# Performance work log

Measured on AMD Instinct MI355X. Metric: run time of the kernel, lower is better.

Reference implementation:

```python
import jax, jax.numpy as jnp
import numpy as np

E = 8        # num_experts
H = 2048     # hidden_size
I = 1408     # expert_intermediate_size
SI = 2816    # shared intermediate = I * num_shared_experts
K = 2        # top_k


def swiglu(x):
    a, b = jnp.split(x, 2, axis=-1)
    return jax.nn.silu(a) * b


def setup_inputs() -> dict:
    key = jax.random.key(0)
    ks = jax.random.split(key, 8)
    hidden_states = jax.random.normal(ks[0], (2, 2048, H), dtype=jnp.float32)
    topk_weight = jax.random.uniform(ks[1], (2, 2048, K), dtype=jnp.float32)
    topk_idx = jax.random.randint(ks[2], (2, 2048, K), 0, E)
    s = 0.02
    W1 = jax.random.normal(ks[3], (E, H, 2 * I), dtype=jnp.float32) * s   # per-expert h->2i (swiglu)
    W2 = jax.random.normal(ks[4], (E, I, H), dtype=jnp.float32) * s      # per-expert i->h
    Ws1 = jax.random.normal(ks[5], (H, 2 * SI), dtype=jnp.float32) * s   # shared h->2*si
    Ws2 = jax.random.normal(ks[6], (SI, H), dtype=jnp.float32) * s       # shared si->h
    return {"hidden_states": hidden_states, "topk_weight": topk_weight,
            "W1": W1, "W2": W2, "Ws1": Ws1, "Ws2": Ws2, "topk_idx": topk_idx}


def reference(hidden_states, topk_weight, W1, W2, Ws1, Ws2, topk_idx):
    orig_shape = hidden_states.shape
    x = hidden_states.reshape(-1, H)                       # [T, h]
    T = x.shape[0]
    # run every expert on every token (dense, faithful to masked-loop math)
    h1 = jnp.einsum('th,ehf->tef', x, W1)                  # [T, E, 2i]
    act = swiglu(h1)                                       # [T, E, i]
    expert_out = jnp.einsum('tei,eih->teh', act, W2)       # [T, E, h]
    # combine weights: comb[t,e] = sum_j topk_weight[t,j] * 1[topk_idx[t,j]==e]
    onehot = jax.nn.one_hot(topk_idx.reshape(T, K), E, dtype=x.dtype)  # [T, K, E]
    comb = jnp.einsum('tk,tke->te', topk_weight.reshape(T, K), onehot)
    y = jnp.einsum('te,teh->th', comb, expert_out)         # [T, h]
    # shared experts MLP on identity
    y = y + swiglu(x @ Ws1) @ Ws2
    return y.reshape(orig_shape)
```

## Files before the change

kernel.cpp:

```cpp
#include <hip/hip_runtime.h>
#include <cmath>

#define E_    8
#define H_    2048
#define IH    1408
#define I2    2816
#define SIH   2816
#define SI2   5632
#define KTOP  2
#define T_    4096
#define NA    (T_*KTOP)
#define MAXR  (NA + E_*256)

typedef __attribute__((ext_vector_type(4)))  short  short4v;
typedef __attribute__((ext_vector_type(8)))  __bf16 bf16x8;
typedef __attribute__((ext_vector_type(4)))  float  f32x4;
typedef unsigned short bf16r;

__device__ __forceinline__ bf16r f2b(float f) {
    unsigned int u = __float_as_uint(f);
    return (bf16r)((u + 0x7FFFu + ((u >> 16) & 1u)) >> 16);
}
__device__ __forceinline__ float b2f(bf16r s) {
    return __uint_as_float(((unsigned int)s) << 16);
}

__device__ __forceinline__ void gld16(const bf16r* g, void* l) {
    __builtin_amdgcn_global_load_lds((const __attribute__((address_space(1))) void*)g,
                                     (__attribute__((address_space(3))) void*)l, 16, 0, 0);
}
__device__ __forceinline__ void barrier_raw() { asm volatile("s_barrier" ::: "memory"); }
template<int N> __device__ __forceinline__ void vmwait() {
    asm volatile("s_waitcnt vmcnt(%0)" :: "i"(N) : "memory");
}

__global__ void route_k(const int* __restrict__ idx, const float* __restrict__ tw,
                        int* __restrict__ route) {
    __shared__ int cnt[E_], cur[E_], offs[E_ + 1];
    int t = threadIdx.x;
    if (t < E_) { cnt[t] = 0; cur[t] = 0; }
    float* wrow = (float*)(route + 64 + MAXR);
    int* pos = route + 64 + 2 * MAXR;
    for (int i = t; i < MAXR; i += 256) { route[64 + i] = -1; wrow[i] = 0.f; }
    __syncthreads();
    for (int a = t; a < NA; a += 256) atomicAdd(&cnt[idx[a]], 1);
    __syncthreads();
    if (t == 0) {
        int run = 0;
        for (int e = 0; e < E_; e++) { offs[e] = run; run += ((cnt[e] + 255) >> 8) << 8; }
        offs[E_] = run;
    }
    __syncthreads();
    for (int a = t; a < NA; a += 256) {
        int e = idx[a];
        int p = atomicAdd(&cur[e], 1);
        int r = offs[e] + p;
        route[64 + r] = a / KTOP;
        wrow[r] = tw[a];
        pos[a] = r;
    }
    if (t <= E_) route[32 + t] = offs[t];
}

__global__ void cvt_k(const float* __restrict__ in, bf16r* __restrict__ out, int n4) {
    int i = blockIdx.x * 256 + threadIdx.x;
    if (i < n4) {
        float4 v = ((const float4*)in)[i];
        short4v o;
        o[0] = (short)f2b(v.x); o[1] = (short)f2b(v.y);
        o[2] = (short)f2b(v.z); o[3] = (short)f2b(v.w);
        ((short4v*)out)[i] = o;
    }
}

__global__ void tconv_k(const float* __restrict__ in, bf16r* __restrict__ out,
                        int R, int C, long ims, long oms) {
    __shared__ bf16r tile[64][65];
    const float* inp = in + blockIdx.z * ims;
    bf16r* outp = out + blockIdx.z * oms;
    int c0 = blockIdx.x * 64, r0 = blockIdx.y * 64;
    int tx = threadIdx.x, ty = threadIdx.y;
    #pragma unroll
    for (int j = 0; j < 16; j++) {
        int r = ty * 16 + j;
        tile[r][tx] = f2b(inp[(long)(r0 + r) * C + c0 + tx]);
    }
    __syncthreads();
    #pragma unroll
    for (int j = 0; j < 16; j++) {
        int c = ty * 16 + j;
        outp[(long)(c0 + c) * R + r0 + tx] = tile[tx][c];
    }
}

__global__ void comb_k(float* __restrict__ out, const bf16r* __restrict__ outR,
                       const int* __restrict__ pos) {
    int i = blockIdx.x * 256 + threadIdx.x;
    int t  = i >> 9;
    int c4 = i & 511;
    int p0 = pos[2 * t], p1 = pos[2 * t + 1];
    float4 o = ((float4*)out)[i];
    short4v r0 = ((const short4v*)(outR + (long)p0 * H_))[c4];
    short4v r1 = ((const short4v*)(outR + (long)p1 * H_))[c4];
    o.x += b2f((bf16r)r0[0]) + b2f((bf16r)r1[0]);
    o.y += b2f((bf16r)r0[1]) + b2f((bf16r)r1[1]);
    o.z += b2f((bf16r)r0[2]) + b2f((bf16r)r1[2]);
    o.w += b2f((bf16r)r0[3]) + b2f((bf16r)r1[3]);
    ((float4*)out)[i] = o;
}


#define PH_READ_A(MH) { _Pragma("unroll") for (int i4 = 0; i4 < 4; i4++) \
                        _Pragma("unroll") for (int kk = 0; kk < 2; kk++) \
                            af[(MH)][i4][kk] = rdA(cur, (MH), i4, kk); }
#define PH_READ_B(NH) { _Pragma("unroll") for (int j2 = 0; j2 < NJ2; j2++) \
                        _Pragma("unroll") for (int kk = 0; kk < 2; kk++) \
                            bfr[(NH)][j2][kk] = rdB(cur, (NH), j2, kk); }
#define PH_MMA(MH, NH) { __builtin_amdgcn_s_setprio(1); \
    _Pragma("unroll") for (int i4 = 0; i4 < 4; i4++) \
    _Pragma("unroll") for (int j2 = 0; j2 < NJ2; j2++) \
    _Pragma("unroll") for (int kk = 0; kk < 2; kk++) \
        acc[(MH)][(NH)][i4][j2] = __builtin_amdgcn_mfma_f32_16x16x32_bf16( \
            af[(MH)][i4][kk], bfr[(NH)][j2][kk], acc[(MH)][(NH)][i4][j2], 0, 0, 0); \
    __builtin_amdgcn_s_setprio(0); }

template<int BNv, int KD, bool GATHER, bool ROUTED, bool PAIRED, int EPI>
__global__ __launch_bounds__(512, 2)
void g8_k(const bf16r* __restrict__ A,
          const bf16r* __restrict__ Bt, long bstride, int F,
          void* __restrict__ Cv, int ldc,
          const int* __restrict__ off, const int* __restrict__ perm,
          const float* __restrict__ wrow, int gM)
{
    constexpr int NJ2 = BNv / 128;
    constexpr int LB  = NJ2;
    constexpr int BHE = BNv * 32;
    constexpr int NT  = KD / 64;
    constexpr int VW  = 4 + 2 * LB;
    static_assert(!PAIRED || NJ2 == 2, "paired swiglu needs BN=256");
    static_assert(NT >= 4 && (NT & 1) == 0, "even K-tile count >= 4");

    extern __shared__ __align__(16) char smem[];
    bf16r* lA = (bf16r*)smem;
    bf16r* lB = (bf16r*)(smem + 65536);

    int nwg = gridDim.x, orig = blockIdx.x;
    int q8 = nwg >> 3, r8 = nwg & 7, xc = orig & 7, o8 = orig >> 3;
    int wgid = (xc < r8 ? xc * (q8 + 1) : r8 * (q8 + 1) + (xc - r8) * q8) + o8;
    int mt = wgid % gM, nt = wgid / gM;
    const int r0 = mt * 256;
    int e = 0;
    if (ROUTED) {
        if (r0 >= off[E_]) return;
        while (e + 1 < E_ && off[e + 1] <= r0) e++;
    }
    const bf16r* Bte = ROUTED ? Bt + (long)e * bstride : Bt;

    const int tid  = threadIdx.x;
    const int lane = tid & 63;
    const int wave = tid >> 6;
    const int wm = wave >> 2, wn = wave & 3;
    const int ml = lane & 15, kg = lane >> 4;
    const int srw  = lane >> 3;
    const int ksrc = ((lane & 7) ^ srw) * 8;

    const bf16r* pA[2][2];
    #pragma unroll
    for (int h = 0; h < 2; h++)
        #pragma unroll
        for (int l = 0; l < 2; l++) {
            int gr = r0 + h * 128 + (wave + 8 * l) * 8 + srw;
            long rw = gr;
            if (GATHER) { int tk = perm[gr]; rw = (tk < 0) ? 0 : tk; }
            pA[h][l] = A + rw * (long)KD + ksrc;
        }
    const bf16r* pB[2][LB];
    #pragma unroll
    for (int nh = 0; nh < 2; nh++)
        #pragma unroll
        for (int l = 0; l < LB; l++) {
            int lr = (wave + 8 * l) * 8 + srw;
            long gr;
            if (PAIRED) {
                int wn_ = lr >> 5, j2_ = (lr >> 4) & 1, ml_ = lr & 15;
                gr = (long)(nt * 128 + nh * 64 + wn_ * 16 + ml_) + (j2_ ? (long)F : 0L);
            } else if (NJ2 == 2) gr = (long)(nt * 256 + nh * 128 + lr);
            else                 gr = (long)(nt * 128 + nh * 64  + lr);
            pB[nh][l] = Bte + gr * (long)KD + ksrc;
        }

    auto stgA = [&](int b, int h, int kp) {
        char* d = smem + ((b * 2 + h) << 14) + (wave << 10);
        gld16(pA[h][0] + kp, d);
        gld16(pA[h][1] + kp, d + 8192);
    };
    auto stgB = [&](int b, int nh, int kp) {
        char* d = smem + 65536 + (b * 2 + nh) * (BHE * 2) + (wave << 10);
        gld16(pB[nh][0] + kp, d);
        if constexpr (LB == 2) gld16(pB[nh][1] + kp, d + 8192);
    };
    auto rdA = [&](int b, int mh, int i4, int kk) -> bf16x8 {
        int row = wm * 64 + i4 * 16 + ml;
        int u = kk * 4 + kg;
        int ee = ((b * 2 + mh) << 13) + row * 64 + ((u ^ (row & 7)) << 3);
        return *(const bf16x8*)&lA[ee];
    };
    auto rdB = [&](int b, int nh, int j2, int kk) -> bf16x8 {
        int rb = (NJ2 == 2) ? (wn * 32 + j2 * 16 + ml) : (wn * 16 + ml);
        int u = kk * 4 + kg;
        int ee = (b * 2 + nh) * BHE + rb * 64 + ((u ^ (rb & 7)) << 3);
        return *(const bf16x8*)&lB[ee];
    };

    f32x4 acc[2][2][4][NJ2];
    #pragma unroll
    for (int a0 = 0; a0 < 2; a0++)
        #pragma unroll
        for (int b0 = 0; b0 < 2; b0++)
            #pragma unroll
            for (int i = 0; i < 4; i++)
                #pragma unroll
                for (int j = 0; j < NJ2; j++)
                    acc[a0][b0][i][j] = f32x4{0.f, 0.f, 0.f, 0.f};

    bf16x8 af[2][4][2], bfr[2][NJ2][2];

    vmwait<0>();
    stgA(0, 0, 0); stgB(0, 0, 0); stgB(0, 1, 0); stgA(0, 1, 0);
    stgA(1, 0, 64); stgB(1, 0, 64);
    vmwait<LB + 2>(); barrier_raw();

    #pragma unroll 2
    for (int t = 0; t < NT; t++) {
        const int cur = t & 1, nxt = cur ^ 1;
        const int k1 = ((t + 1 < NT) ? (t + 1) : (NT - 1)) * 64;
        const int k2 = ((t + 2 < NT) ? (t + 2) : (NT - 1)) * 64;
        PH_READ_A(0); PH_READ_B(0);
        stgB(nxt, 1, k1);
        vmwait<VW>();
        barrier_raw();
        PH_MMA(0, 0);
        barrier_raw();
        PH_READ_B(1);
        stgA(nxt, 1, k1);
        vmwait<VW>();
        barrier_raw();
        PH_MMA(0, 1);
        barrier_raw();
        PH_READ_A(1);
        stgA(cur, 0, k2);
        barrier_raw();
        PH_MMA(1, 0);
        barrier_raw();
        stgB(cur, 0, k2);
        vmwait<VW>();
        barrier_raw();
        PH_MMA(1, 1);
        barrier_raw();
    }
    vmwait<0>();

    const long colbase = (long)nt * (PAIRED ? 128 : BNv);
    #pragma unroll
    for (int mh = 0; mh < 2; mh++)
        #pragma unroll
        for (int i4 = 0; i4 < 4; i4++)
            #pragma unroll
            for (int rr = 0; rr < 4; rr++) {
                long row = (long)r0 + mh * 128 + wm * 64 + i4 * 16 + kg * 4 + rr;
                if constexpr (PAIRED) {
                    bf16r* ap = (bf16r*)Cv + row * (long)ldc + colbase;
                    #pragma unroll
                    for (int nh = 0; nh < 2; nh++) {
                        float g = acc[mh][nh][i4][0][rr];
                        float u = acc[mh][nh][i4][1][rr];
                        float s = g / (1.0f + __expf(-g));
                        ap[nh * 64 + wn * 16 + ml] = f2b(s * u);
                    }
                } else if constexpr (EPI == 1) {
                    float* cp = (float*)Cv + row * (long)ldc + colbase;
                    #pragma unroll
                    for (int nh = 0; nh < 2; nh++)
                        #pragma unroll
                        for (int j2 = 0; j2 < NJ2; j2++)
                            cp[nh * (BNv / 2) + wn * (BNv / 8) + j2 * 16 + ml] =
                                acc[mh][nh][i4][j2][rr];
                } else {
                    int tok = perm[row];
                    if (tok >= 0) {
                        float w = wrow[row];
                        bf16r* cp = (bf16r*)Cv + row * (long)ldc + colbase;
                        #pragma unroll
                        for (int nh = 0; nh < 2; nh++)
                            #pragma unroll
                            for (int j2 = 0; j2 < NJ2; j2++)
                                cp[nh * (BNv / 2) + wn * (BNv / 8) + j2 * 16 + ml] =
                                    f2b(w * acc[mh][nh][i4][j2][rr]);
                    }
                }
            }
}

#undef PH_READ_A
#undef PH_READ_B
#undef PH_MMA

extern "C" void kernel_launch(void* const* d_in, const int* in_sizes, int n_in,
                              void* d_out, int out_size, void* d_ws, size_t ws_size,
                              hipStream_t stream)
{
    const float* x   = (const float*)d_in[0];
    const float* tw  = (const float*)d_in[1];
    const float* W1  = (const float*)d_in[2];
    const float* W2  = (const float*)d_in[3];
    const float* Ws1 = (const float*)d_in[4];
    const float* Ws2 = (const float*)d_in[5];
    const int*   tix = (const int*)d_in[6];
    float* out = (float*)d_out;

    char* ws    = (char*)d_ws;
    int*  route = (int*)ws;
    const int*   off  = route + 32;
    const int*   perm = route + 64;
    const float* wrow = (const float*)(route + 64 + MAXR);
    const int*   pos  = route + 64 + 2 * MAXR;

    bf16r* xb   = (bf16r*)(ws + (1u << 20));
    bf16r* W1t  = xb   + (size_t)T_ * H_;
    bf16r* W2t  = W1t  + (size_t)E_ * I2 * H_;
    bf16r* Ws1t = W2t  + (size_t)E_ * H_ * IH;
    bf16r* Ws2t = Ws1t + (size_t)SI2 * H_;
    bf16r* actS = Ws2t + (size_t)H_ * SIH;
    bf16r* actR = actS + (size_t)T_ * SIH;
    bf16r* outR = W1t;

    static bool attr_done = false;
    if (!attr_done) {
        hipFuncSetAttribute(reinterpret_cast<const void*>(&g8_k<256,2048,false,false,true,0>),
                            hipFuncAttributeMaxDynamicSharedMemorySize, 131072);
        hipFuncSetAttribute(reinterpret_cast<const void*>(&g8_k<256,2048,true,true,true,0>),
                            hipFuncAttributeMaxDynamicSharedMemorySize, 131072);
        hipFuncSetAttribute(reinterpret_cast<const void*>(&g8_k<128,2816,false,false,false,1>),
                            hipFuncAttributeMaxDynamicSharedMemorySize, 98304);
        hipFuncSetAttribute(reinterpret_cast<const void*>(&g8_k<256,1408,false,true,false,2>),
                            hipFuncAttributeMaxDynamicSharedMemorySize, 131072);
        attr_done = true;
    }

    route_k<<<1, 256, 0, stream>>>(tix, tw, route);

    cvt_k<<<(T_ * H_ / 4 + 255) / 256, 256, 0, stream>>>(x, xb, T_ * H_ / 4);
    tconv_k<<<dim3(SI2 / 64, H_ / 64, 1), dim3(64, 4), 0, stream>>>(Ws1, Ws1t, H_, SI2, 0, 0);
    tconv_k<<<dim3(H_ / 64, SIH / 64, 1), dim3(64, 4), 0, stream>>>(Ws2, Ws2t, SIH, H_, 0, 0);
    tconv_k<<<dim3(I2 / 64, H_ / 64, E_), dim3(64, 4), 0, stream>>>(W1, W1t, H_, I2,
                                                                    (long)H_ * I2, (long)I2 * H_);
    tconv_k<<<dim3(H_ / 64, IH / 64, E_), dim3(64, 4), 0, stream>>>(W2, W2t, IH, H_,
                                                                    (long)IH * H_, (long)H_ * IH);

    g8_k<256,2048,false,false,true,0><<<dim3((SIH/128)*(T_/256)), dim3(512), 131072, stream>>>(
        xb, Ws1t, 0, SIH, actS, SIH, nullptr, nullptr, nullptr, T_/256);
    g8_k<128,2816,false,false,false,1><<<dim3((H_/128)*(T_/256)), dim3(512), 98304, stream>>>(
        actS, Ws2t, 0, 0, out, H_, nullptr, nullptr, nullptr, T_/256);
    g8_k<256,2048,true,true,true,0><<<dim3((IH/128)*(MAXR/256)), dim3(512), 131072, stream>>>(
        xb, W1t, (long)I2 * H_, IH, actR, IH, off, perm, nullptr, MAXR/256);
    g8_k<256,1408,false,true,false,2><<<dim3((H_/256)*(MAXR/256)), dim3(512), 131072, stream>>>(
        actR, W2t, (long)H_ * IH, 0, outR, H_, off, perm, wrow, MAXR/256);
    comb_k<<<T_ * H_ / 4 / 256, 256, 0, stream>>>(out, outR, pos);
}
```

Baseline: 816.7 us.

## Merge shared and routed GEMMs into combined launches; vectorize weight transpose

Fuses the shared-expert and routed-expert GEMMs of each stage into a single grid launch that branches on block index, so the two independent problems fill the GPU together and launch gaps disappear. The weight transpose-convert kernel is rewritten to use float4 loads and 16-byte bf16 stores with a padded tile. Routing and gather flags become runtime values, and the block-swizzle formula drops its remainder handling, which assumes each grid count is a multiple of 8. The shared second GEMM now requests the larger 128KB LDS budget, which may limit occupancy.

```diff
diff --git a/kernel.cpp b/kernel.cpp
--- a/kernel.cpp
+++ b/kernel.cpp
@@ -11,6 +11,11 @@
 #define T_    4096
 #define NA    (T_*KTOP)
 #define MAXR  (NA + E_*256)
+
+#define NS1   ((SIH/128)*(T_/256))
+#define NR1   ((IH/128)*(MAXR/256))
+#define NS2   ((H_/128)*(T_/256))
+#define NR2   ((H_/256)*(MAXR/256))
 
 typedef __attribute__((ext_vector_type(4)))  short  short4v;
 typedef __attribute__((ext_vector_type(8)))  __bf16 bf16x8;
@@ -73,24 +78,29 @@
     }
 }
 
-__global__ void tconv_k(const float* __restrict__ in, bf16r* __restrict__ out,
-                        int R, int C, long ims, long oms) {
-    __shared__ bf16r tile[64][65];
+__global__ void tconv2_k(const float* __restrict__ in, bf16r* __restrict__ out,
+                         int R, int C, long ims, long oms) {
+    __shared__ bf16r tile[64][72];
     const float* inp = in + blockIdx.z * ims;
     bf16r* outp = out + blockIdx.z * oms;
     int c0 = blockIdx.x * 64, r0 = blockIdx.y * 64;
-    int tx = threadIdx.x, ty = threadIdx.y;
+    int t = threadIdx.x;
+    int tc4 = (t & 15) * 4;
+    int tr  = t >> 4;
     #pragma unroll
-    for (int j = 0; j < 16; j++) {
-        int r = ty * 16 + j;
-        tile[r][tx] = f2b(inp[(long)(r0 + r) * C + c0 + tx]);
+    for (int j = 0; j < 2; j++) {
+        int r = tr + j * 32;
+        float4 v = *(const float4*)&inp[(long)(r0 + r) * C + c0 + tc4];
+        tile[tc4 + 0][r] = f2b(v.x);
+        tile[tc4 + 1][r] = f2b(v.y);
+        tile[tc4 + 2][r] = f2b(v.z);
+        tile[tc4 + 3][r] = f2b(v.w);
     }
     __syncthreads();
-    #pragma unroll
-    for (int j = 0; j < 16; j++) {
-        int c = ty * 16 + j;
-        outp[(long)(c0 + c) * R + r0 + tx] = tile[tx][c];
-    }
+    int oc = t >> 3;
+    int seg = t & 7;
+    bf16x8 o = *(const bf16x8*)&tile[oc][seg * 8];
+    *(bf16x8*)&outp[(long)(c0 + oc) * R + r0 + seg * 8] = o;
 }
 
 __global__ void comb_k(float* __restrict__ out, const bf16r* __restrict__ outR,
@@ -124,13 +134,14 @@
             af[(MH)][i4][kk], bfr[(NH)][j2][kk], acc[(MH)][(NH)][i4][j2], 0, 0, 0); \
     __builtin_amdgcn_s_setprio(0); }
 
-template<int BNv, int KD, bool GATHER, bool ROUTED, bool PAIRED, int EPI>
-__global__ __launch_bounds__(512, 2)
-void g8_k(const bf16r* __restrict__ A,
-          const bf16r* __restrict__ Bt, long bstride, int F,
-          void* __restrict__ Cv, int ldc,
-          const int* __restrict__ off, const int* __restrict__ perm,
-          const float* __restrict__ wrow, int gM)
+template<int BNv, int KD, bool PAIRED, int EPI>
+__device__ __forceinline__ void g8_body(
+    int sub, int nwg, int gM, bool routed, bool gather,
+    const bf16r* __restrict__ A,
+    const bf16r* __restrict__ Bt, long bstride, int F,
+    void* __restrict__ Cv, int ldc,
+    const int* __restrict__ off, const int* __restrict__ perm,
+    const float* __restrict__ wrow)
 {
     constexpr int NJ2 = BNv / 128;
     constexpr int LB  = NJ2;
@@ -144,17 +155,16 @@
     bf16r* lA = (bf16r*)smem;
     bf16r* lB = (bf16r*)(smem + 65536);
 
-    int nwg = gridDim.x, orig = blockIdx.x;
-    int q8 = nwg >> 3, r8 = nwg & 7, xc = orig & 7, o8 = orig >> 3;
-    int wgid = (xc < r8 ? xc * (q8 + 1) : r8 * (q8 + 1) + (xc - r8) * q8) + o8;
+    int q8 = nwg >> 3, xc = sub & 7, o8 = sub >> 3;
+    int wgid = xc * q8 + o8;
     int mt = wgid % gM, nt = wgid / gM;
     const int r0 = mt * 256;
     int e = 0;
-    if (ROUTED) {
+    if (routed) {
         if (r0 >= off[E_]) return;
         while (e + 1 < E_ && off[e + 1] <= r0) e++;
     }
-    const bf16r* Bte = ROUTED ? Bt + (long)e * bstride : Bt;
+    const bf16r* Bte = routed ? Bt + (long)e * bstride : Bt;
 
     const int tid  = threadIdx.x;
     const int lane = tid & 63;
@@ -171,7 +181,7 @@
         for (int l = 0; l < 2; l++) {
             int gr = r0 + h * 128 + (wave + 8 * l) * 8 + srw;
             long rw = gr;
-            if (GATHER) { int tk = perm[gr]; rw = (tk < 0) ? 0 : tk; }
+            if (gather) { int tk = perm[gr]; rw = (tk < 0) ? 0 : tk; }
             pA[h][l] = A + rw * (long)KD + ksrc;
         }
     const bf16r* pB[2][LB];
@@ -305,6 +315,48 @@
 #undef PH_READ_B
 #undef PH_MMA
 
+__global__ __launch_bounds__(512, 2)
+void g1m_k(const bf16r* __restrict__ xb,
+           const bf16r* __restrict__ Ws1t, bf16r* __restrict__ actS,
+           const bf16r* __restrict__ W1t,  bf16r* __restrict__ actR,
+           const int* __restrict__ route)
+{
+    const int* off  = route + 32;
+    const int* perm = route + 64;
+    int orig = blockIdx.x;
+    bool rt = orig >= NS1;
+    int sub  = rt ? orig - NS1 : orig;
+    int nwg  = rt ? NR1 : NS1;
+    int gM   = rt ? MAXR / 256 : T_ / 256;
+    const bf16r* B = rt ? W1t : Ws1t;
+    long bs  = rt ? (long)I2 * H_ : 0;
+    int F    = rt ? IH : SIH;
+    bf16r* C = rt ? actR : actS;
+    int ldc  = rt ? IH : SIH;
+    g8_body<256, 2048, true, 0>(sub, nwg, gM, rt, rt, xb, B, bs, F, C, ldc,
+                                off, perm, nullptr);
+}
+
+__global__ __launch_bounds__(512, 2)
+void g2m_k(const bf16r* __restrict__ actS, const bf16r* __restrict__ Ws2t,
+           float* __restrict__ out,
+           const bf16r* __restrict__ actR, const bf16r* __restrict__ W2t,
+           bf16r* __restrict__ outR,
+           const int* __restrict__ route)
+{
+    const int* off  = route + 32;
+    const int* perm = route + 64;
+    const float* wrow = (const float*)(route + 64 + MAXR);
+    int orig = blockIdx.x;
+    if (orig < NS2) {
+        g8_body<128, 2816, false, 1>(orig, NS2, T_ / 256, false, false,
+                                     actS, Ws2t, 0, 0, out, H_, off, perm, nullptr);
+    } else {
+        g8_body<256, 1408, false, 2>(orig - NS2, NR2, MAXR / 256, true, false,
+                                     actR, W2t, (long)H_ * IH, 0, outR, H_, off, perm, wrow);
+    }
+}
+
 extern "C" void kernel_launch(void* const* d_in, const int* in_sizes, int n_in,
                               void* d_out, int out_size, void* d_ws, size_t ws_size,
                               hipStream_t stream)
@@ -320,10 +372,7 @@
 
     char* ws    = (char*)d_ws;
     int*  route = (int*)ws;
-    const int*   off  = route + 32;
-    const int*   perm = route + 64;
-    const float* wrow = (const float*)(route + 64 + MAXR);
-    const int*   pos  = route + 64 + 2 * MAXR;
+    const int* pos = route + 64 + 2 * MAXR;
 
     bf16r* xb   = (bf16r*)(ws + (1u << 20));
     bf16r* W1t  = xb   + (size_t)T_ * H_;
@@ -336,13 +385,9 @@
 
     static bool attr_done = false;
     if (!attr_done) {
-        hipFuncSetAttribute(reinterpret_cast<const void*>(&g8_k<256,2048,false,false,true,0>),
+        hipFuncSetAttribute(reinterpret_cast<const void*>(&g1m_k),
                             hipFuncAttributeMaxDynamicSharedMemorySize, 131072);
-        hipFuncSetAttribute(reinterpret_cast<const void*>(&g8_k<256,2048,true,true,true,0>),
-                            hipFuncAttributeMaxDynamicSharedMemorySize, 131072);
-        hipFuncSetAttribute(reinterpret_cast<const void*>(&g8_k<128,2816,false,false,false,1>),
-                            hipFuncAttributeMaxDynamicSharedMemorySize, 98304);
-        hipFuncSetAttribute(reinterpret_cast<const void*>(&g8_k<256,1408,false,true,false,2>),
+        hipFuncSetAttribute(reinterpret_cast<const void*>(&g2m_k),
                             hipFuncAttributeMaxDynamicSharedMemorySize, 131072);
         attr_done = true;
     }
@@ -350,20 +395,14 @@
     route_k<<<1, 256, 0, stream>>>(tix, tw, route);
 
     cvt_k<<<(T_ * H_ / 4 + 255) / 256, 256, 0, stream>>>(x, xb, T_ * H_ / 4);
-    tconv_k<<<dim3(SI2 / 64, H_ / 64, 1), dim3(64, 4), 0, stream>>>(Ws1, Ws1t, H_, SI2, 0, 0);
-    tconv_k<<<dim3(H_ / 64, SIH / 64, 1), dim3(64, 4), 0, stream>>>(Ws2, Ws2t, SIH, H_, 0, 0);
-    tconv_k<<<dim3(I2 / 64, H_ / 64, E_), dim3(64, 4), 0, stream>>>(W1, W1t, H_, I2,
-                                                                    (long)H_ * I2, (long)I2 * H_);
-    tconv_k<<<dim3(H_ / 64, IH / 64, E_), dim3(64, 4), 0, stream>>>(W2, W2t, IH, H_,
-                                                                    (long)IH * H_, (long)H_ * IH);
-
-    g8_k<256,2048,false,false,true,0><<<dim3((SIH/128)*(T_/256)), dim3(512), 131072, stream>>>(
-        xb, Ws1t, 0, SIH, actS, SIH, nullptr, nullptr, nullptr, T_/256);
-    g8_k<128,2816,false,false,false,1><<<dim3((H_/128)*(T_/256)), dim3(512), 98304, stream>>>(
-        actS, Ws2t, 0, 0, out, H_, nullptr, nullptr, nullptr, T_/256);
-    g8_k<256,2048,true,true,true,0><<<dim3((IH/128)*(MAXR/256)), dim3(512), 131072, stream>>>(
-        xb, W1t, (long)I2 * H_, IH, actR, IH, off, perm, nullptr, MAXR/256);
-    g8_k<256,1408,false,true,false,2><<<dim3((H_/256)*(MAXR/256)), dim3(512), 131072, stream>>>(
-        actR, W2t, (long)H_ * IH, 0, outR, H_, off, perm, wrow, MAXR/256);
+    tconv2_k<<<dim3(SI2 / 64, H_ / 64, 1), 512, 0, stream>>>(Ws1, Ws1t, H_, SI2, 0, 0);
+    tconv2_k<<<dim3(H_ / 64, SIH / 64, 1), 512, 0, stream>>>(Ws2, Ws2t, SIH, H_, 0, 0);
+    tconv2_k<<<dim3(I2 / 64, H_ / 64, E_), 512, 0, stream>>>(W1, W1t, H_, I2,
+                                                             (long)H_ * I2, (long)I2 * H_);
+    tconv2_k<<<dim3(H_ / 64, IH / 64, E_), 512, 0, stream>>>(W2, W2t, IH, H_,
+                                                             (long)IH * H_, (long)H_ * IH);
+
+    g1m_k<<<dim3(NS1 + NR1), dim3(512), 131072, stream>>>(xb, Ws1t, actS, W1t, actR, route);
+    g2m_k<<<dim3(NS2 + NR2), dim3(512), 131072, stream>>>(actS, Ws2t, out, actR, W2t, outR, route);
     comb_k<<<T_ * H_ / 4 / 256, 256, 0, stream>>>(out, outR, pos);
 }
```

Result: faster. 748.6 us (-8.3%).
